# Performance work log

Measured on AMD Instinct MI355X. Metric: run time of the kernel, lower is better.

The kernel has to match this reference:

```python
import jax, jax.numpy as jnp
import numpy as np

N, E, B = 10000, 60000, 4
NODE_IN, EDGE_IN, COND_IN, SCALE_IN = 6, 6, 10, 4
H, KW, OUT = 64, 256, 1
NUM_LAYERS = 3


def _lin(key, fan_in, fan_out):
    return jax.random.normal(key, (fan_in, fan_out), jnp.float32) / np.sqrt(fan_in).astype(np.float32)


def setup_inputs() -> dict:
    key = jax.random.key(0)
    ks = jax.random.split(key, 16)
    return {
        "x": jax.random.normal(ks[0], (N, NODE_IN), jnp.float32),
        "edge_attr": jax.random.normal(ks[1], (E, EDGE_IN), jnp.float32),
        "conditions": jax.random.normal(ks[2], (B, COND_IN), jnp.float32),
        "scale": jax.random.normal(ks[3], (B, SCALE_IN), jnp.float32),
        "edge_index": jax.random.randint(ks[4], (2, E), 0, N, dtype=jnp.int32),
        "batch": jnp.sort(jax.random.randint(ks[5], (N,), 0, B, dtype=jnp.int32)),
        # node encoder
        "nW1": _lin(ks[6], NODE_IN, H), "nb1": jnp.zeros((H,), jnp.float32),
        "nW2": _lin(ks[7], H, H), "nb2": jnp.zeros((H,), jnp.float32),
        # condition encoder
        "cW1": _lin(ks[8], COND_IN + SCALE_IN, H), "cb1": jnp.zeros((H,), jnp.float32),
        "cW2": _lin(ks[9], H, H), "cb2": jnp.zeros((H,), jnp.float32),
        # kernel network (DenseNet [EDGE_IN+H, KW//2, KW, H*H])
        "kW1": _lin(ks[10], EDGE_IN + H, KW // 2), "kb1": jnp.zeros((KW // 2,), jnp.float32),
        "kW2": _lin(ks[11], KW // 2, KW), "kb2": jnp.zeros((KW,), jnp.float32),
        "kW3": _lin(ks[12], KW, H * H), "kb3": jnp.zeros((H * H,), jnp.float32),
        # NNConv root weight + bias
        "root": _lin(ks[13], H, H), "conv_bias": jnp.zeros((H,), jnp.float32),
        # output head
        "oW": _lin(ks[14], H, OUT), "ob": jnp.zeros((OUT,), jnp.float32),
    }


def reference(x, edge_attr, conditions, scale, edge_index, batch,
              nW1, nb1, nW2, nb2, cW1, cb1, cW2, cb2,
              kW1, kb1, kW2, kb2, kW3, kb3, root, conv_bias, oW, ob):
    # node + condition encoders
    h = jax.nn.relu(x @ nW1 + nb1) @ nW2 + nb2                                   # [N,H]
    u = jax.nn.relu(jnp.concatenate([conditions, scale], 1) @ cW1 + cb1) @ cW2 + cb2  # [B,H]

    src, dst = edge_index[0], edge_index[1]
    # per-edge conditioned attributes
    ea = jnp.concatenate([edge_attr, u[batch[src]]], axis=1)                     # [E,EDGE_IN+H]
    # kernel network -> per-edge H x H weight (same every layer, compute once)
    k = jax.nn.relu(ea @ kW1 + kb1)
    k = jax.nn.relu(k @ kW2 + kb2)
    w = (k @ kW3 + kb3).reshape(E, H, H)                                          # [E,H,H]

    # mean-aggregation degree (clamped to >=1, matching scatter_mean semantics)
    deg = jnp.maximum(jax.ops.segment_sum(jnp.ones((E,), x.dtype), dst, num_segments=N), 1.0)

    for _ in range(NUM_LAYERS):
        msg = jnp.einsum('ei,eio->eo', h[src], w)                                 # gather + bmm
        agg = jax.ops.segment_sum(msg, dst, num_segments=N) / deg[:, None]        # scatter-mean
        h = jax.nn.relu(agg + h @ root + conv_bias)

    out = h @ oW + ob                                                             # [N,OUT]
    return out, u
```

## Files before the change

kernel.cpp:

```cpp
#include <hip/hip_runtime.h>
#include <hip/hip_fp16.h>

#define N_NODES 10000
#define NPAD    10016
#define N_EDGES 60000
#define EPAD    60032

typedef _Float16 f16;
typedef f16 f16x8 __attribute__((ext_vector_type(8)));
typedef f16 f16x2 __attribute__((ext_vector_type(2)));
typedef float f32x4 __attribute__((ext_vector_type(4)));

#define SV2(v, j) __builtin_shufflevector(v, v, 2 * (j), 2 * (j) + 1)

#if __has_builtin(__builtin_amdgcn_fdot2)
__device__ __forceinline__ float FDOT2(f16x2 a, f16x2 b, float c) {
    return __builtin_amdgcn_fdot2(a, b, c, false);
}
#else
__device__ __forceinline__ float FDOT2(f16x2 a, f16x2 b, float c) {
    return c + (float)a[0] * (float)b[0] + (float)a[1] * (float)b[1];
}
#endif

__global__ void k_node_enc(const float* __restrict__ x, const float* __restrict__ W1,
                           const float* __restrict__ b1, const float* __restrict__ W2,
                           const float* __restrict__ b2, float* __restrict__ h,
                           f16* __restrict__ h16) {
    __shared__ float t[4][64];
    int g = threadIdx.x >> 6, j = threadIdx.x & 63;
    int node = blockIdx.x * 4 + g;
    float acc = b1[j];
#pragma unroll
    for (int i = 0; i < 6; ++i) acc += x[node * 6 + i] * W1[i * 64 + j];
    t[g][j] = fmaxf(acc, 0.f);
    __syncthreads();
    float acc2 = b2[j];
#pragma unroll
    for (int i = 0; i < 64; ++i) acc2 += t[g][i] * W2[i * 64 + j];
    h[node * 64 + j] = acc2;
    h16[node * 64 + j] = (f16)acc2;
}

__global__ void k_cond_enc(const float* __restrict__ cond, const float* __restrict__ scl,
                           const float* __restrict__ W1, const float* __restrict__ b1,
                           const float* __restrict__ W2, const float* __restrict__ b2,
                           float* __restrict__ u, float* __restrict__ out_u) {
    __shared__ float t[4][64];
    __shared__ float cat[4][14];
    int g = threadIdx.x >> 6, j = threadIdx.x & 63;
    if (threadIdx.x < 56) {
        int b = threadIdx.x / 14, i = threadIdx.x % 14;
        cat[b][i] = (i < 10) ? cond[b * 10 + i] : scl[b * 4 + (i - 10)];
    }
    __syncthreads();
    float acc = b1[j];
#pragma unroll
    for (int i = 0; i < 14; ++i) acc += cat[g][i] * W1[i * 64 + j];
    t[g][j] = fmaxf(acc, 0.f);
    __syncthreads();
    float acc2 = b2[j];
#pragma unroll
    for (int i = 0; i < 64; ++i) acc2 += t[g][i] * W2[i * 64 + j];
    u[g * 64 + j] = acc2;
    out_u[g * 64 + j] = acc2;
}

__global__ void k_deg(const int* __restrict__ dst, float* __restrict__ deg) {
    int e = blockIdx.x * 256 + threadIdx.x;
    if (e < N_EDGES) atomicAdd(&deg[dst[e]], 1.0f);
}
__global__ void k_deg_inv(float* __restrict__ deg) {
    int n = blockIdx.x * 256 + threadIdx.x;
    if (n < N_NODES) deg[n] = 1.0f / fmaxf(deg[n], 1.0f);
}

__global__ void k_csr_count(const int* __restrict__ src, int* __restrict__ cnt) {
    int e = blockIdx.x * 256 + threadIdx.x;
    if (e < N_EDGES) atomicAdd(&cnt[src[e]], 1);
}
__global__ void k_csr_scan(const int* __restrict__ cnt, int* __restrict__ srcPtr,
                           int* __restrict__ cursor) {
    __shared__ int part[256];
    int t = threadIdx.x;
    int base = t * 40;
    int s = 0;
#pragma unroll 1
    for (int i = 0; i < 40; ++i) { int idx = base + i; if (idx < NPAD) s += cnt[idx]; }
    part[t] = s;
    __syncthreads();
    if (t == 0) {
        int run = 0;
        for (int i = 0; i < 256; ++i) { int v = part[i]; part[i] = run; run += v; }
    }
    __syncthreads();
    int run = part[t];
#pragma unroll 1
    for (int i = 0; i < 40; ++i) {
        int idx = base + i;
        if (idx <= NPAD) {
            srcPtr[idx] = run; cursor[idx] = run;
            if (idx < NPAD) run += cnt[idx];
        }
    }
}
__global__ void k_csr_fill(const int* __restrict__ src, int* __restrict__ cursor,
                           int* __restrict__ srcIdx) {
    int e = blockIdx.x * 256 + threadIdx.x;
    if (e < N_EDGES) { int p = atomicAdd(&cursor[src[e]], 1); srcIdx[p] = e; }
}

__global__ void k_mp2(const float* __restrict__ kW3, f16* __restrict__ Mp2) {
    int k = threadIdx.x, o = blockIdx.x, ib = blockIdx.y;
#pragma unroll
    for (int j = 0; j < 8; ++j) {
        int i = ib * 8 + j;
        Mp2[((size_t)o * 256 + k) * 64 + i] = (f16)kW3[(size_t)k * 4096 + i * 64 + o];
    }
}

__global__ void k_hb(const float* __restrict__ h, const float* __restrict__ kb3,
                     float* __restrict__ hb) {
    __shared__ float t[4][64];
    int g = threadIdx.x >> 6, j = threadIdx.x & 63;
    int node = blockIdx.x * 4 + g;
    t[g][j] = h[node * 64 + j];
    __syncthreads();
    float acc = 0.f;
#pragma unroll
    for (int i = 0; i < 64; ++i) acc += t[g][i] * kb3[i * 64 + j];
    hb[node * 64 + j] = acc;
}

__global__ __launch_bounds__(256) void k_edge12(const float* __restrict__ ea, const int* __restrict__ ei,
                                                const int* __restrict__ batch, const float* __restrict__ u,
                                                const float* __restrict__ W1, const float* __restrict__ b1,
                                                const float* __restrict__ W2, const float* __restrict__ b2,
                                                f16* __restrict__ k2) {
    __shared__ float u_s[256];
    __shared__ float ea_s[16][6];
    __shared__ int b_s[16];
    __shared__ float k1_s[16][128];
    int tid = threadIdx.x;
    int e0 = blockIdx.x * 16;
    u_s[tid] = u[tid];
    if (tid < 96) {
        int e = tid / 6, i = tid % 6;
        int eg = e0 + e;
        ea_s[e][i] = (eg < N_EDGES) ? ea[(size_t)eg * 6 + i] : 0.f;
    }
    if (tid < 16) {
        int eg = e0 + tid;
        b_s[tid] = (eg < N_EDGES) ? batch[ei[eg]] : 0;
    }
    __syncthreads();
    int j = tid & 127;
#pragma unroll 1
    for (int p = 0; p < 8; ++p) {
        int e = p * 2 + (tid >> 7);
        float acc = b1[j];
#pragma unroll
        for (int i = 0; i < 6; ++i) acc += ea_s[e][i] * W1[i * 128 + j];
        const float* ur = u_s + b_s[e] * 64;
#pragma unroll
        for (int i = 0; i < 64; ++i) acc += ur[i] * W1[(6 + i) * 128 + j];
        k1_s[e][j] = fmaxf(acc, 0.f);
    }
    __syncthreads();
    float acc2[16];
#pragma unroll
    for (int e = 0; e < 16; ++e) acc2[e] = b2[tid];
    for (int i = 0; i < 128; ++i) {
        float w = W2[(size_t)i * 256 + tid];
#pragma unroll
        for (int e = 0; e < 16; ++e) acc2[e] += k1_s[e][i] * w;
    }
#pragma unroll
    for (int e = 0; e < 16; ++e) {
        int eg = e0 + e;
        k2[(size_t)eg * 256 + tid] = (f16)((eg < N_EDGES) ? fmaxf(acc2[e], 0.f) : 0.f);
    }
}

__global__ __launch_bounds__(256) void k_gmsg(const f16* __restrict__ k2, const f16* __restrict__ Mp2,
                                              const f16* __restrict__ h16, const float* __restrict__ hb,
                                              const int* __restrict__ ei, const int* __restrict__ srcPtr,
                                              const int* __restrict__ srcIdx, const float* __restrict__ dinv,
                                              float* __restrict__ agg) {
    __shared__ __align__(16) f16 G[16 * 8 * 256];
    char* Gb = (char*)G;
    int tid = threadIdx.x, wave = tid >> 6, lane = tid & 63;
    int n0 = blockIdx.x * 16;
    int og = blockIdx.y;
    f16x8 a0 = *(const f16x8*)(h16 + (size_t)(n0 + (lane & 15)) * 64 + (lane >> 4) * 8);
    f16x8 a1 = *(const f16x8*)(h16 + (size_t)(n0 + (lane & 15)) * 64 + 32 + (lane >> 4) * 8);
    const f16* Brow = Mp2 + ((size_t)og * 2048 + wave * 512 + (lane & 15)) * 64 + (lane >> 4) * 8;
    f16x8 p0a = *(const f16x8*)(Brow);
    f16x8 p0b = *(const f16x8*)(Brow + 32);
    f16x8 p1a = *(const f16x8*)(Brow + 1024);
    f16x8 p1b = *(const f16x8*)(Brow + 1024 + 32);
#pragma unroll 1
    for (int nf = 0; nf < 32; ++nf) {
        f16x8 c0 = p0a, c1 = p0b;
        p0a = p1a; p0b = p1b;
        if (nf < 30) {
            p1a = *(const f16x8*)(Brow + (nf + 2) * 1024);
            p1b = *(const f16x8*)(Brow + (nf + 2) * 1024 + 32);
        }
        f32x4 acc = {};
        acc = __builtin_amdgcn_mfma_f32_16x16x32_f16(a0, c0, acc, 0, 0, 0);
        acc = __builtin_amdgcn_mfma_f32_16x16x32_f16(a1, c1, acc, 0, 0, 0);
        int olocal = wave * 2 + (nf >> 4);
        int kk = ((nf & 15) << 4) + (lane & 15);
        int gq = kk >> 3, grb = (kk & 7) * 2;
#pragma unroll
        for (int jj = 0; jj < 4; ++jj) {
            int ro = ((lane >> 4) * 4 + jj) * 8 + olocal;
            *(f16*)(Gb + ro * 512 + ((gq ^ (ro & 31)) << 4) + grb) = (f16)acc[jj];
        }
    }
    __syncthreads();
    int sp0 = srcPtr[n0];
    int cnt8 = (srcPtr[n0 + 16] - sp0) << 3;
#pragma unroll 1
    for (int p = tid; p < cnt8; p += 256) {
        int e = srcIdx[sp0 + (p >> 3)];
        int o = p & 7;
        int sn = ei[e];
        int ro = (sn - n0) * 8 + o, s = ro & 31;
        const char* gbase = Gb + ro * 512;
        const f16* kp = k2 + (size_t)e * 256;
        float m0 = 0.f, m1 = 0.f, m2 = 0.f, m3 = 0.f;
        float m4 = 0.f, m5 = 0.f, m6 = 0.f, m7 = 0.f;
#define CHUNK(kc, M) { f16x8 kv = *(const f16x8*)(kp + (kc) * 8); \
        f16x8 gv = *(const f16x8*)(gbase + (((kc) ^ s) << 4)); \
        M = FDOT2(SV2(kv, 0), SV2(gv, 0), M); M = FDOT2(SV2(kv, 1), SV2(gv, 1), M); \
        M = FDOT2(SV2(kv, 2), SV2(gv, 2), M); M = FDOT2(SV2(kv, 3), SV2(gv, 3), M); }
        CHUNK(0, m0)  CHUNK(1, m1)  CHUNK(2, m2)  CHUNK(3, m3)
        CHUNK(4, m4)  CHUNK(5, m5)  CHUNK(6, m6)  CHUNK(7, m7)
        CHUNK(8, m0)  CHUNK(9, m1)  CHUNK(10, m2) CHUNK(11, m3)
        CHUNK(12, m4) CHUNK(13, m5) CHUNK(14, m6) CHUNK(15, m7)
        CHUNK(16, m0) CHUNK(17, m1) CHUNK(18, m2) CHUNK(19, m3)
        CHUNK(20, m4) CHUNK(21, m5) CHUNK(22, m6) CHUNK(23, m7)
        CHUNK(24, m0) CHUNK(25, m1) CHUNK(26, m2) CHUNK(27, m3)
        CHUNK(28, m4) CHUNK(29, m5) CHUNK(30, m6) CHUNK(31, m7)
#undef CHUNK
        float m = ((m0 + m1) + (m2 + m3)) + ((m4 + m5) + (m6 + m7));
        int ogo = (og << 3) + o;
        int d = ei[N_EDGES + e];
        atomicAdd(&agg[(size_t)d * 64 + ogo], (m + hb[(size_t)sn * 64 + ogo]) * dinv[d]);
    }
}

__global__ void k_update(const float* __restrict__ agg, const float* __restrict__ h,
                         const float* __restrict__ root, const float* __restrict__ bias,
                         float* __restrict__ hn, f16* __restrict__ hn16) {
    __shared__ float t[4][64];
    int g = threadIdx.x >> 6, j = threadIdx.x & 63;
    int node = blockIdx.x * 4 + g;
    t[g][j] = h[node * 64 + j];
    __syncthreads();
    float acc = agg[node * 64 + j] + bias[j];
#pragma unroll
    for (int i = 0; i < 64; ++i) acc += t[g][i] * root[i * 64 + j];
    float v = fmaxf(acc, 0.f);
    hn[node * 64 + j] = v;
    hn16[node * 64 + j] = (f16)v;
}

__global__ void k_out(const float* __restrict__ h, const float* __restrict__ oW,
                      const float* __restrict__ ob, float* __restrict__ out) {
    int wg = (blockIdx.x * 256 + threadIdx.x) >> 6;
    int lane = threadIdx.x & 63;
    if (wg >= N_NODES) return;
    float p = h[wg * 64 + lane] * oW[lane];
#pragma unroll
    for (int s = 32; s > 0; s >>= 1) p += __shfl_xor(p, s);
    if (lane == 0) out[wg] = p + ob[0];
}

__global__ void k_sentinel(float* out) { out[0] = 1e30f; }

extern "C" void kernel_launch(void* const* d_in, const int* in_sizes, int n_in,
                              void* d_out, int out_size, void* d_ws, size_t ws_size,
                              hipStream_t stream) {
    const float* x          = (const float*)d_in[0];
    const float* edge_attr  = (const float*)d_in[1];
    const float* conditions = (const float*)d_in[2];
    const float* scale      = (const float*)d_in[3];
    const int*   edge_index = (const int*)d_in[4];
    const int*   batch      = (const int*)d_in[5];
    const float* nW1 = (const float*)d_in[6];  const float* nb1 = (const float*)d_in[7];
    const float* nW2 = (const float*)d_in[8];  const float* nb2 = (const float*)d_in[9];
    const float* cW1 = (const float*)d_in[10]; const float* cb1 = (const float*)d_in[11];
    const float* cW2 = (const float*)d_in[12]; const float* cb2 = (const float*)d_in[13];
    const float* kW1 = (const float*)d_in[14]; const float* kb1 = (const float*)d_in[15];
    const float* kW2 = (const float*)d_in[16]; const float* kb2 = (const float*)d_in[17];
    const float* kW3 = (const float*)d_in[18]; const float* kb3 = (const float*)d_in[19];
    const float* root = (const float*)d_in[20]; const float* conv_bias = (const float*)d_in[21];
    const float* oW  = (const float*)d_in[22]; const float* ob  = (const float*)d_in[23];
    float* out = (float*)d_out;

    char* ws = (char*)d_ws;
    size_t off = 0;
    auto alloc = [&](size_t bytes) -> char* {
        char* p = ws + off;
        off += (bytes + 255) & ~(size_t)255;
        return p;
    };
    float* h_a   = (float*)alloc((size_t)N_NODES * 64 * 4);
    float* h_b   = (float*)alloc((size_t)N_NODES * 64 * 4);
    f16*   h16_a = (f16*)alloc((size_t)NPAD * 64 * 2);
    f16*   h16_b = (f16*)alloc((size_t)NPAD * 64 * 2);
    float* agg   = (float*)alloc((size_t)N_NODES * 64 * 4);
    float* hb    = (float*)alloc((size_t)N_NODES * 64 * 4);
    float* u     = (float*)alloc(256 * 4);
    float* deg   = (float*)alloc((size_t)N_NODES * 4);
    int*   cnt   = (int*)alloc((size_t)NPAD * 4);
    int*   srcPtr= (int*)alloc((size_t)(NPAD + 1) * 4);
    int*   cursor= (int*)alloc((size_t)(NPAD + 1) * 4);
    int*   srcIdx= (int*)alloc((size_t)N_EDGES * 4);
    f16*   k2    = (f16*)alloc((size_t)EPAD * 256 * 2);
    f16*   Mp2   = (f16*)alloc((size_t)16384 * 64 * 2);

    if (off > ws_size) {
        k_sentinel<<<1, 1, 0, stream>>>(out);
        return;
    }

    hipMemsetAsync(deg, 0, (size_t)N_NODES * 4, stream);
    hipMemsetAsync(cnt, 0, (size_t)NPAD * 4, stream);
    k_node_enc<<<2500, 256, 0, stream>>>(x, nW1, nb1, nW2, nb2, h_a, h16_a);
    k_cond_enc<<<1, 256, 0, stream>>>(conditions, scale, cW1, cb1, cW2, cb2, u, out + N_NODES);
    k_deg<<<(N_EDGES + 255) / 256, 256, 0, stream>>>(edge_index + N_EDGES, deg);
    k_deg_inv<<<(N_NODES + 255) / 256, 256, 0, stream>>>(deg);
    k_csr_count<<<(N_EDGES + 255) / 256, 256, 0, stream>>>(edge_index, cnt);
    k_csr_scan<<<1, 256, 0, stream>>>(cnt, srcPtr, cursor);
    k_csr_fill<<<(N_EDGES + 255) / 256, 256, 0, stream>>>(edge_index, cursor, srcIdx);
    k_mp2<<<dim3(64, 8), 256, 0, stream>>>(kW3, Mp2);
    k_edge12<<<EPAD / 16, 256, 0, stream>>>(edge_attr, edge_index, batch, u, kW1, kb1, kW2, kb2, k2);

    float* hc = h_a; float* hn = h_b;
    f16* hc16 = h16_a; f16* hn16 = h16_b;
    for (int l = 0; l < 3; ++l) {
        hipMemsetAsync(agg, 0, (size_t)N_NODES * 64 * 4, stream);
        k_hb<<<2500, 256, 0, stream>>>(hc, kb3, hb);
        k_gmsg<<<dim3(NPAD / 16, 8), 256, 0, stream>>>(k2, Mp2, hc16, hb, edge_index,
                                                       srcPtr, srcIdx, deg, agg);
        k_update<<<2500, 256, 0, stream>>>(agg, hc, root, conv_bias, hn, hn16);
        float* tf = hc; hc = hn; hn = tf;
        f16* t16 = hc16; hc16 = hn16; hn16 = t16;
    }
    k_out<<<2500, 256, 0, stream>>>(hc, oW, ob, out);
}
```

Before: 955.6 us.

## Fuse hb into encoder/update, merge degree counts, restructure gmsg per-thread work

Folds the hb = h·kb3 projection into the node encoder and update kernels, removing the separate k_hb launch each layer. Agg is zeroed inside k_update instead of by a memset per layer, and the degree and CSR counts are merged into one kernel with a single memset. In k_gmsg each thread now computes four outputs per edge, reusing the loaded k2 vectors four times, and the grid is reordered so the output-group index varies fastest. This cuts redundant global loads of k2 and launch overhead, at the cost of more registers per thread and less parallelism per block.

```diff
diff --git a/kernel.cpp b/kernel.cpp
--- a/kernel.cpp
+++ b/kernel.cpp
@@ -25,9 +25,11 @@
 
 __global__ void k_node_enc(const float* __restrict__ x, const float* __restrict__ W1,
                            const float* __restrict__ b1, const float* __restrict__ W2,
-                           const float* __restrict__ b2, float* __restrict__ h,
-                           f16* __restrict__ h16) {
+                           const float* __restrict__ b2, const float* __restrict__ kb3,
+                           float* __restrict__ h, f16* __restrict__ h16,
+                           float* __restrict__ hb) {
     __shared__ float t[4][64];
+    __shared__ float t2[4][64];
     int g = threadIdx.x >> 6, j = threadIdx.x & 63;
     int node = blockIdx.x * 4 + g;
     float acc = b1[j];
@@ -40,6 +42,12 @@
     for (int i = 0; i < 64; ++i) acc2 += t[g][i] * W2[i * 64 + j];
     h[node * 64 + j] = acc2;
     h16[node * 64 + j] = (f16)acc2;
+    t2[g][j] = acc2;
+    __syncthreads();
+    float hbv = 0.f;
+#pragma unroll
+    for (int i = 0; i < 64; ++i) hbv += t2[g][i] * kb3[i * 64 + j];
+    hb[node * 64 + j] = hbv;
 }
 
 __global__ void k_cond_enc(const float* __restrict__ cond, const float* __restrict__ scl,
@@ -66,19 +74,19 @@
     out_u[g * 64 + j] = acc2;
 }
 
-__global__ void k_deg(const int* __restrict__ dst, float* __restrict__ deg) {
+__global__ void k_degcnt(const int* __restrict__ ei, float* __restrict__ deg,
+                         int* __restrict__ cnt) {
     int e = blockIdx.x * 256 + threadIdx.x;
-    if (e < N_EDGES) atomicAdd(&deg[dst[e]], 1.0f);
+    if (e < N_EDGES) {
+        atomicAdd(&deg[ei[N_EDGES + e]], 1.0f);
+        atomicAdd(&cnt[ei[e]], 1);
+    }
 }
 __global__ void k_deg_inv(float* __restrict__ deg) {
     int n = blockIdx.x * 256 + threadIdx.x;
     if (n < N_NODES) deg[n] = 1.0f / fmaxf(deg[n], 1.0f);
 }
 
-__global__ void k_csr_count(const int* __restrict__ src, int* __restrict__ cnt) {
-    int e = blockIdx.x * 256 + threadIdx.x;
-    if (e < N_EDGES) atomicAdd(&cnt[src[e]], 1);
-}
 __global__ void k_csr_scan(const int* __restrict__ cnt, int* __restrict__ srcPtr,
                            int* __restrict__ cursor) {
     __shared__ int part[256];
@@ -117,19 +125,6 @@
         int i = ib * 8 + j;
         Mp2[((size_t)o * 256 + k) * 64 + i] = (f16)kW3[(size_t)k * 4096 + i * 64 + o];
     }
-}
-
-__global__ void k_hb(const float* __restrict__ h, const float* __restrict__ kb3,
-                     float* __restrict__ hb) {
-    __shared__ float t[4][64];
-    int g = threadIdx.x >> 6, j = threadIdx.x & 63;
-    int node = blockIdx.x * 4 + g;
-    t[g][j] = h[node * 64 + j];
-    __syncthreads();
-    float acc = 0.f;
-#pragma unroll
-    for (int i = 0; i < 64; ++i) acc += t[g][i] * kb3[i * 64 + j];
-    hb[node * 64 + j] = acc;
 }
 
 __global__ __launch_bounds__(256) void k_edge12(const float* __restrict__ ea, const int* __restrict__ ei,
@@ -190,8 +185,8 @@
     __shared__ __align__(16) f16 G[16 * 8 * 256];
     char* Gb = (char*)G;
     int tid = threadIdx.x, wave = tid >> 6, lane = tid & 63;
-    int n0 = blockIdx.x * 16;
-    int og = blockIdx.y;
+    int og = blockIdx.x;
+    int n0 = blockIdx.y * 16;
     f16x8 a0 = *(const f16x8*)(h16 + (size_t)(n0 + (lane & 15)) * 64 + (lane >> 4) * 8);
     f16x8 a1 = *(const f16x8*)(h16 + (size_t)(n0 + (lane & 15)) * 64 + 32 + (lane >> 4) * 8);
     const f16* Brow = Mp2 + ((size_t)og * 2048 + wave * 512 + (lane & 15)) * 64 + (lane >> 4) * 8;
@@ -221,51 +216,84 @@
     }
     __syncthreads();
     int sp0 = srcPtr[n0];
-    int cnt8 = (srcPtr[n0 + 16] - sp0) << 3;
-#pragma unroll 1
-    for (int p = tid; p < cnt8; p += 256) {
-        int e = srcIdx[sp0 + (p >> 3)];
-        int o = p & 7;
+    int cnt2 = (srcPtr[n0 + 16] - sp0) << 1;
+#pragma unroll 1
+    for (int p = tid; p < cnt2; p += 256) {
+        int e = srcIdx[sp0 + (p >> 1)];
+        int oq = p & 1;
         int sn = ei[e];
-        int ro = (sn - n0) * 8 + o, s = ro & 31;
-        const char* gbase = Gb + ro * 512;
+        int d = ei[N_EDGES + e];
+        int rb = (sn - n0) * 8 + oq * 4;
+        const char* g0 = Gb + (size_t)(rb + 0) * 512; int s0 = (rb + 0) & 31;
+        const char* g1 = Gb + (size_t)(rb + 1) * 512; int s1 = (rb + 1) & 31;
+        const char* g2 = Gb + (size_t)(rb + 2) * 512; int s2 = (rb + 2) & 31;
+        const char* g3 = Gb + (size_t)(rb + 3) * 512; int s3 = (rb + 3) & 31;
         const f16* kp = k2 + (size_t)e * 256;
         float m0 = 0.f, m1 = 0.f, m2 = 0.f, m3 = 0.f;
-        float m4 = 0.f, m5 = 0.f, m6 = 0.f, m7 = 0.f;
-#define CHUNK(kc, M) { f16x8 kv = *(const f16x8*)(kp + (kc) * 8); \
-        f16x8 gv = *(const f16x8*)(gbase + (((kc) ^ s) << 4)); \
-        M = FDOT2(SV2(kv, 0), SV2(gv, 0), M); M = FDOT2(SV2(kv, 1), SV2(gv, 1), M); \
-        M = FDOT2(SV2(kv, 2), SV2(gv, 2), M); M = FDOT2(SV2(kv, 3), SV2(gv, 3), M); }
-        CHUNK(0, m0)  CHUNK(1, m1)  CHUNK(2, m2)  CHUNK(3, m3)
-        CHUNK(4, m4)  CHUNK(5, m5)  CHUNK(6, m6)  CHUNK(7, m7)
-        CHUNK(8, m0)  CHUNK(9, m1)  CHUNK(10, m2) CHUNK(11, m3)
-        CHUNK(12, m4) CHUNK(13, m5) CHUNK(14, m6) CHUNK(15, m7)
-        CHUNK(16, m0) CHUNK(17, m1) CHUNK(18, m2) CHUNK(19, m3)
-        CHUNK(20, m4) CHUNK(21, m5) CHUNK(22, m6) CHUNK(23, m7)
-        CHUNK(24, m0) CHUNK(25, m1) CHUNK(26, m2) CHUNK(27, m3)
-        CHUNK(28, m4) CHUNK(29, m5) CHUNK(30, m6) CHUNK(31, m7)
-#undef CHUNK
-        float m = ((m0 + m1) + (m2 + m3)) + ((m4 + m5) + (m6 + m7));
-        int ogo = (og << 3) + o;
-        int d = ei[N_EDGES + e];
-        atomicAdd(&agg[(size_t)d * 64 + ogo], (m + hb[(size_t)sn * 64 + ogo]) * dinv[d]);
-    }
-}
-
-__global__ void k_update(const float* __restrict__ agg, const float* __restrict__ h,
+#pragma unroll
+        for (int kb = 0; kb < 32; kb += 8) {
+            f16x8 kv[8];
+#pragma unroll
+            for (int c = 0; c < 8; ++c) kv[c] = *(const f16x8*)(kp + (kb + c) * 8);
+#pragma unroll
+            for (int c = 0; c < 8; ++c) {
+                int kc = kb + c;
+                f16x8 gv0 = *(const f16x8*)(g0 + ((kc ^ s0) << 4));
+                m0 = FDOT2(SV2(kv[c], 0), SV2(gv0, 0), m0);
+                m0 = FDOT2(SV2(kv[c], 1), SV2(gv0, 1), m0);
+                m0 = FDOT2(SV2(kv[c], 2), SV2(gv0, 2), m0);
+                m0 = FDOT2(SV2(kv[c], 3), SV2(gv0, 3), m0);
+                f16x8 gv1 = *(const f16x8*)(g1 + ((kc ^ s1) << 4));
+                m1 = FDOT2(SV2(kv[c], 0), SV2(gv1, 0), m1);
+                m1 = FDOT2(SV2(kv[c], 1), SV2(gv1, 1), m1);
+                m1 = FDOT2(SV2(kv[c], 2), SV2(gv1, 2), m1);
+                m1 = FDOT2(SV2(kv[c], 3), SV2(gv1, 3), m1);
+                f16x8 gv2 = *(const f16x8*)(g2 + ((kc ^ s2) << 4));
+                m2 = FDOT2(SV2(kv[c], 0), SV2(gv2, 0), m2);
+                m2 = FDOT2(SV2(kv[c], 1), SV2(gv2, 1), m2);
+                m2 = FDOT2(SV2(kv[c], 2), SV2(gv2, 2), m2);
+                m2 = FDOT2(SV2(kv[c], 3), SV2(gv2, 3), m2);
+                f16x8 gv3 = *(const f16x8*)(g3 + ((kc ^ s3) << 4));
+                m3 = FDOT2(SV2(kv[c], 0), SV2(gv3, 0), m3);
+                m3 = FDOT2(SV2(kv[c], 1), SV2(gv3, 1), m3);
+                m3 = FDOT2(SV2(kv[c], 2), SV2(gv3, 2), m3);
+                m3 = FDOT2(SV2(kv[c], 3), SV2(gv3, 3), m3);
+            }
+        }
+        int ogo = (og << 3) + (oq << 2);
+        float dv = dinv[d];
+        const float* hp = hb + (size_t)sn * 64 + ogo;
+        float* ap = agg + (size_t)d * 64 + ogo;
+        atomicAdd(ap + 0, (m0 + hp[0]) * dv);
+        atomicAdd(ap + 1, (m1 + hp[1]) * dv);
+        atomicAdd(ap + 2, (m2 + hp[2]) * dv);
+        atomicAdd(ap + 3, (m3 + hp[3]) * dv);
+    }
+}
+
+__global__ void k_update(float* __restrict__ agg, const float* __restrict__ h,
                          const float* __restrict__ root, const float* __restrict__ bias,
-                         float* __restrict__ hn, f16* __restrict__ hn16) {
+                         const float* __restrict__ kb3, float* __restrict__ hn,
+                         f16* __restrict__ hn16, float* __restrict__ hb) {
     __shared__ float t[4][64];
     int g = threadIdx.x >> 6, j = threadIdx.x & 63;
     int node = blockIdx.x * 4 + g;
     t[g][j] = h[node * 64 + j];
     __syncthreads();
     float acc = agg[node * 64 + j] + bias[j];
+    agg[node * 64 + j] = 0.f;
 #pragma unroll
     for (int i = 0; i < 64; ++i) acc += t[g][i] * root[i * 64 + j];
     float v = fmaxf(acc, 0.f);
     hn[node * 64 + j] = v;
     hn16[node * 64 + j] = (f16)v;
+    __syncthreads();
+    t[g][j] = v;
+    __syncthreads();
+    float hbv = 0.f;
+#pragma unroll
+    for (int i = 0; i < 64; ++i) hbv += t[g][i] * kb3[i * 64 + j];
+    hb[node * 64 + j] = hbv;
 }
 
 __global__ void k_out(const float* __restrict__ h, const float* __restrict__ oW,
@@ -308,33 +336,33 @@
         off += (bytes + 255) & ~(size_t)255;
         return p;
     };
-    float* h_a   = (float*)alloc((size_t)N_NODES * 64 * 4);
-    float* h_b   = (float*)alloc((size_t)N_NODES * 64 * 4);
-    f16*   h16_a = (f16*)alloc((size_t)NPAD * 64 * 2);
-    f16*   h16_b = (f16*)alloc((size_t)NPAD * 64 * 2);
-    float* agg   = (float*)alloc((size_t)N_NODES * 64 * 4);
-    float* hb    = (float*)alloc((size_t)N_NODES * 64 * 4);
-    float* u     = (float*)alloc(256 * 4);
-    float* deg   = (float*)alloc((size_t)N_NODES * 4);
-    int*   cnt   = (int*)alloc((size_t)NPAD * 4);
-    int*   srcPtr= (int*)alloc((size_t)(NPAD + 1) * 4);
-    int*   cursor= (int*)alloc((size_t)(NPAD + 1) * 4);
-    int*   srcIdx= (int*)alloc((size_t)N_EDGES * 4);
-    f16*   k2    = (f16*)alloc((size_t)EPAD * 256 * 2);
-    f16*   Mp2   = (f16*)alloc((size_t)16384 * 64 * 2);
+    float* h_a    = (float*)alloc((size_t)N_NODES * 64 * 4);
+    float* h_b    = (float*)alloc((size_t)N_NODES * 64 * 4);
+    f16*   h16_a  = (f16*)alloc((size_t)NPAD * 64 * 2);
+    f16*   h16_b  = (f16*)alloc((size_t)NPAD * 64 * 2);
+    float* agg    = (float*)alloc((size_t)N_NODES * 64 * 4);
+    float* hb     = (float*)alloc((size_t)N_NODES * 64 * 4);
+    float* u      = (float*)alloc(256 * 4);
+    float* degcnt = (float*)alloc((size_t)2 * NPAD * 4);
+    float* deg    = degcnt;
+    int*   cnt    = (int*)(degcnt + NPAD);
+    int*   srcPtr = (int*)alloc((size_t)(NPAD + 1) * 4);
+    int*   cursor = (int*)alloc((size_t)(NPAD + 1) * 4);
+    int*   srcIdx = (int*)alloc((size_t)N_EDGES * 4);
+    f16*   k2     = (f16*)alloc((size_t)EPAD * 256 * 2);
+    f16*   Mp2    = (f16*)alloc((size_t)16384 * 64 * 2);
 
     if (off > ws_size) {
         k_sentinel<<<1, 1, 0, stream>>>(out);
         return;
     }
 
-    hipMemsetAsync(deg, 0, (size_t)N_NODES * 4, stream);
-    hipMemsetAsync(cnt, 0, (size_t)NPAD * 4, stream);
-    k_node_enc<<<2500, 256, 0, stream>>>(x, nW1, nb1, nW2, nb2, h_a, h16_a);
+    hipMemsetAsync(degcnt, 0, (size_t)2 * NPAD * 4, stream);
+    hipMemsetAsync(agg, 0, (size_t)N_NODES * 64 * 4, stream);
+    k_node_enc<<<2500, 256, 0, stream>>>(x, nW1, nb1, nW2, nb2, kb3, h_a, h16_a, hb);
     k_cond_enc<<<1, 256, 0, stream>>>(conditions, scale, cW1, cb1, cW2, cb2, u, out + N_NODES);
-    k_deg<<<(N_EDGES + 255) / 256, 256, 0, stream>>>(edge_index + N_EDGES, deg);
+    k_degcnt<<<(N_EDGES + 255) / 256, 256, 0, stream>>>(edge_index, deg, cnt);
     k_deg_inv<<<(N_NODES + 255) / 256, 256, 0, stream>>>(deg);
-    k_csr_count<<<(N_EDGES + 255) / 256, 256, 0, stream>>>(edge_index, cnt);
     k_csr_scan<<<1, 256, 0, stream>>>(cnt, srcPtr, cursor);
     k_csr_fill<<<(N_EDGES + 255) / 256, 256, 0, stream>>>(edge_index, cursor, srcIdx);
     k_mp2<<<dim3(64, 8), 256, 0, stream>>>(kW3, Mp2);
@@ -343,11 +371,9 @@
     float* hc = h_a; float* hn = h_b;
     f16* hc16 = h16_a; f16* hn16 = h16_b;
     for (int l = 0; l < 3; ++l) {
-        hipMemsetAsync(agg, 0, (size_t)N_NODES * 64 * 4, stream);
-        k_hb<<<2500, 256, 0, stream>>>(hc, kb3, hb);
-        k_gmsg<<<dim3(NPAD / 16, 8), 256, 0, stream>>>(k2, Mp2, hc16, hb, edge_index,
+        k_gmsg<<<dim3(8, NPAD / 16), 256, 0, stream>>>(k2, Mp2, hc16, hb, edge_index,
                                                        srcPtr, srcIdx, deg, agg);
-        k_update<<<2500, 256, 0, stream>>>(agg, hc, root, conv_bias, hn, hn16);
+        k_update<<<2500, 256, 0, stream>>>(agg, hc, root, conv_bias, kb3, hn, hn16, hb);
         float* tf = hc; hc = hn; hn = tf;
         f16* t16 = hc16; hc16 = hn16; hn16 = t16;
     }
```

Result: slower. 1.161 ms (+21.5%).
